# Kernel optimization log

Hardware: AMD Instinct MI355X
Metric: run time of the kernel (lower is better)

Reference implementation:

```python
import jax, jax.numpy as jnp
import numpy as np

N = 50000      # nodes
E = 1600000    # edges (avg degree 32)
F_IN = 3       # PROTEINS num_node_features
H = 64         # dim_h
G = 512        # num graphs in batch
C = 2          # PROTEINS num_classes
BN_EPS = 1e-5


def setup_inputs() -> dict:
    key = jax.random.key(0)
    ks = iter(jax.random.split(key, 64))

    def rn(shape, s=0.1):
        return (jax.random.normal(next(ks), shape) * s).astype(jnp.float32)

    inp = {"x": rn((N, F_IN), 1.0)}
    for li, din in ((1, F_IN), (2, H), (3, H)):
        p = f"conv{li}_"
        inp[p + "w1"] = rn((din, H))
        inp[p + "b1"] = rn((H,))
        inp[p + "bn_g"] = jnp.ones((H,), jnp.float32)
        inp[p + "bn_b"] = jnp.zeros((H,), jnp.float32)
        inp[p + "bn_m"] = rn((H,))
        inp[p + "bn_v"] = jax.random.uniform(next(ks), (H,), jnp.float32, 0.5, 1.5)
        inp[p + "w2"] = rn((H, H))
        inp[p + "b2"] = rn((H,))
    inp["lin1_w"] = rn((3 * H, 3 * H))
    inp["lin1_b"] = rn((3 * H,))
    inp["lin2_w"] = rn((3 * H, C))
    inp["lin2_b"] = rn((C,))
    inp["edge_index"] = jax.random.randint(next(ks), (2, E), 0, N, jnp.int64)
    inp["batch"] = jnp.sort(jax.random.randint(next(ks), (N,), 0, G, jnp.int64))
    return inp


def gin_conv(x, src, dst, w1, b1, g, bb, m, v, w2, b2):
    # GINConv, eps=0: mlp(x + sum_{j->i} x_j); aggregate messages at target (dst)
    agg = jax.ops.segment_sum(x[src], dst, num_segments=N)  # [N, d]
    h = x + agg
    h = h @ w1 + b1
    h = (h - m) * jax.lax.rsqrt(v + BN_EPS) * g + bb  # BatchNorm1d (eval)
    h = jax.nn.relu(h)
    h = jax.nn.relu(h @ w2 + b2)
    return h


def reference(x,
              conv1_w1, conv1_b1, conv1_bn_g, conv1_bn_b, conv1_bn_m, conv1_bn_v, conv1_w2, conv1_b2,
              conv2_w1, conv2_b1, conv2_bn_g, conv2_bn_b, conv2_bn_m, conv2_bn_v, conv2_w2, conv2_b2,
              conv3_w1, conv3_b1, conv3_bn_g, conv3_bn_b, conv3_bn_m, conv3_bn_v, conv3_w2, conv3_b2,
              lin1_w, lin1_b, lin2_w, lin2_b,
              edge_index, batch):
    src, dst = edge_index[0], edge_index[1]
    h1 = gin_conv(x,  src, dst, conv1_w1, conv1_b1, conv1_bn_g, conv1_bn_b, conv1_bn_m, conv1_bn_v, conv1_w2, conv1_b2)
    h2 = gin_conv(h1, src, dst, conv2_w1, conv2_b1, conv2_bn_g, conv2_bn_b, conv2_bn_m, conv2_bn_v, conv2_w2, conv2_b2)
    h3 = gin_conv(h2, src, dst, conv3_w1, conv3_b1, conv3_bn_g, conv3_bn_b, conv3_bn_m, conv3_bn_v, conv3_w2, conv3_b2)
    # global_add_pool per graph
    p1 = jax.ops.segment_sum(h1, batch, num_segments=G)
    p2 = jax.ops.segment_sum(h2, batch, num_segments=G)
    p3 = jax.ops.segment_sum(h3, batch, num_segments=G)
    h = jnp.concatenate((p1, p2, p3), axis=1)          # [G, 3H]
    h = jax.nn.relu(h @ lin1_w + lin1_b)
    # dropout p=0.5 is identity in eval mode
    h = h @ lin2_w + lin2_b                            # [G, C]
    return (h, jax.nn.log_softmax(h, axis=1))
```

## Files before the change

kernel.cpp:

```cpp
#include <hip/hip_runtime.h>
#include <hip/hip_bf16.h>
#include <math.h>

#define N_NODES 50000
#define N_EDGES 1600000
#define H 64
#define G_GRAPHS 512
#define C_CLS 2
#define BN_EPS 1e-5f
#define NBUCK 196
#define BUCKCAP 16384
#define E4 (N_EDGES / 4)
#define CSR_BLOCKS ((E4 + 511) / 512)
#define IOP 72

typedef __attribute__((ext_vector_type(8))) short short8;
typedef __attribute__((ext_vector_type(4))) float floatx4;

__device__ __forceinline__ float bflo(unsigned int u) { return __uint_as_float(u << 16); }
__device__ __forceinline__ float bfhi(unsigned int u) { return __uint_as_float(u & 0xffff0000u); }
__device__ __forceinline__ unsigned int bf16_rne(float f) {
    unsigned int u = __float_as_uint(f);
    u += 0x7fffu + ((u >> 16) & 1u);
    return u >> 16;
}

__global__ __launch_bounds__(256) void prep_kernel(
    const float* __restrict__ w2_0, const float* __restrict__ w1_1,
    const float* __restrict__ w2_1, const float* __restrict__ w1_2,
    const float* __restrict__ w2_2, unsigned short* __restrict__ wt,
    const float* __restrict__ x, uint2* __restrict__ xb) {
    int b = blockIdx.x, t = threadIdx.x;
    if (b < 5) {
        const float* w = (b == 0) ? w2_0 : (b == 1) ? w1_1 : (b == 2) ? w2_1
                         : (b == 3) ? w1_2 : w2_2;
        unsigned short* o = wt + b * (H * H);
        for (int idx = t; idx < H * H; idx += 256) {
            int k = idx >> 6, j = idx & 63;
            o[j * H + k] = (unsigned short)bf16_rne(w[idx]);
        }
    } else {
        int node = (b - 5) * 256 + t;
        if (node < N_NODES) {
            uint2 p;
            p.x = bf16_rne(x[node * 3 + 0]) | (bf16_rne(x[node * 3 + 1]) << 16);
            p.y = bf16_rne(x[node * 3 + 2]);
            xb[node] = p;
        }
    }
}

__global__ __launch_bounds__(256) void scatter1_kernel(const int* __restrict__ src,
                                                       const int* __restrict__ dst,
                                                       int* __restrict__ gcnt,
                                                       int* __restrict__ gpacked) {
    __shared__ int bh[NBUCK];
    int t = threadIdx.x;
    if (t < NBUCK) bh[t] = 0;
    __syncthreads();
    int base = blockIdx.x * 512;

    int pkA[4], bkA[4], lrA[4]; bool vA = false;
    int pkB[4], bkB[4], lrB[4]; bool vB = false;
    {
        int i = base + t;
        if (i < E4) {
            vA = true;
            int4 s4 = ((const int4*)src)[i];
            int4 d4 = ((const int4*)dst)[i];
            bkA[0] = d4.x >> 8; pkA[0] = ((d4.x & 255) << 16) | s4.x; lrA[0] = atomicAdd(&bh[bkA[0]], 1);
            bkA[1] = d4.y >> 8; pkA[1] = ((d4.y & 255) << 16) | s4.y; lrA[1] = atomicAdd(&bh[bkA[1]], 1);
            bkA[2] = d4.z >> 8; pkA[2] = ((d4.z & 255) << 16) | s4.z; lrA[2] = atomicAdd(&bh[bkA[2]], 1);
            bkA[3] = d4.w >> 8; pkA[3] = ((d4.w & 255) << 16) | s4.w; lrA[3] = atomicAdd(&bh[bkA[3]], 1);
        }
    }
    {
        int i = base + 256 + t;
        if (i < E4) {
            vB = true;
            int4 s4 = ((const int4*)src)[i];
            int4 d4 = ((const int4*)dst)[i];
            bkB[0] = d4.x >> 8; pkB[0] = ((d4.x & 255) << 16) | s4.x; lrB[0] = atomicAdd(&bh[bkB[0]], 1);
            bkB[1] = d4.y >> 8; pkB[1] = ((d4.y & 255) << 16) | s4.y; lrB[1] = atomicAdd(&bh[bkB[1]], 1);
            bkB[2] = d4.z >> 8; pkB[2] = ((d4.z & 255) << 16) | s4.z; lrB[2] = atomicAdd(&bh[bkB[2]], 1);
            bkB[3] = d4.w >> 8; pkB[3] = ((d4.w & 255) << 16) | s4.w; lrB[3] = atomicAdd(&bh[bkB[3]], 1);
        }
    }
    __syncthreads();
    if (t < NBUCK) {
        int c = bh[t];
        bh[t] = c ? atomicAdd(&gcnt[t], c) : 0;
    }
    __syncthreads();
    if (vA) {
#pragma unroll
        for (int q = 0; q < 4; q++) gpacked[bkA[q] * BUCKCAP + bh[bkA[q]] + lrA[q]] = pkA[q];
    }
    if (vB) {
#pragma unroll
        for (int q = 0; q < 4; q++) gpacked[bkB[q] * BUCKCAP + bh[bkB[q]] + lrB[q]] = pkB[q];
    }
}

__global__ __launch_bounds__(256) void bcsr_kernel(const int* __restrict__ gpacked,
                                                   const int* __restrict__ gcnt,
                                                   int* __restrict__ row_start,
                                                   int* __restrict__ edge_src) {
    __shared__ int cnt[256];
    __shared__ int pref[256];
    int b = blockIdx.x;
    int t = threadIdx.x;

    int v = (t < NBUCK) ? gcnt[t] : 0;
    pref[t] = v;
    __syncthreads();
    for (int off = 1; off < 256; off <<= 1) {
        int u = 0;
        if (t >= off) u = pref[t - off];
        __syncthreads();
        if (t >= off) pref[t] += u;
        __syncthreads();
    }
    int bs = (b > 0) ? pref[b - 1] : 0;
    int cnt_b = gcnt[b];
    if (b == 0 && t == 0) row_start[N_NODES] = N_EDGES;
    __syncthreads();

    const int* gp = gpacked + (size_t)b * BUCKCAP;
    cnt[t] = 0;
    __syncthreads();
    for (int i = t; i < cnt_b; i += 256) atomicAdd(&cnt[gp[i] >> 16], 1);
    __syncthreads();
    int c = cnt[t];
    pref[t] = c;
    __syncthreads();
    for (int off = 1; off < 256; off <<= 1) {
        int u = 0;
        if (t >= off) u = pref[t - off];
        __syncthreads();
        if (t >= off) pref[t] += u;
        __syncthreads();
    }
    int excl = pref[t] - c;
    int node = b * 256 + t;
    if (node < N_NODES) row_start[node] = bs + excl;
    cnt[t] = excl;
    __syncthreads();
    for (int i = t; i < cnt_b; i += 256) {
        int p = gp[i];
        int pos = atomicAdd(&cnt[p >> 16], 1);
        edge_src[bs + pos] = p & 0xffff;
    }
}

__global__ __launch_bounds__(512) void gin1_fused16_kernel(
    const float* __restrict__ x, const uint2* __restrict__ xb,
    const int* __restrict__ row_start, const int* __restrict__ edge_src,
    const float* __restrict__ w1, const float* __restrict__ b1,
    const float* __restrict__ bn_g, const float* __restrict__ bn_b,
    const float* __restrict__ bn_m, const float* __restrict__ bn_v,
    const unsigned short* __restrict__ w2t, const float* __restrict__ b2,
    __hip_bfloat16* __restrict__ hout) {
    __shared__ unsigned short s_mid[16 * IOP];

    int tid = threadIdx.x;
    int wave = tid >> 6, j = tid & 63;
    int nodebase = blockIdx.x * 16;

    float wj0 = w1[j], wj1 = w1[H + j], wj2 = w1[2 * H + j];
    float sc = rsqrtf(bn_v[j] + BN_EPS) * bn_g[j];
    float sh = bn_b[j] - bn_m[j] * sc;
    float bj = b1[j];

    for (int nl = wave * 2; nl < wave * 2 + 2; nl++) {
        int node = nodebase + nl;
        int rs = row_start[node], re = row_start[node + 1];
        float a0 = 0.f, a1 = 0.f, a2 = 0.f;
        for (int t = rs + j; t < re; t += 64) {
            uint2 p = xb[edge_src[t]];
            a0 += bflo(p.x); a1 += bfhi(p.x); a2 += bflo(p.y);
        }
#pragma unroll
        for (int off = 32; off > 0; off >>= 1) {
            a0 += __shfl_xor(a0, off);
            a1 += __shfl_xor(a1, off);
            a2 += __shfl_xor(a2, off);
        }
        float in0 = a0 + x[node * 3 + 0];
        float in1 = a1 + x[node * 3 + 1];
        float in2 = a2 + x[node * 3 + 2];
        float m = bj + in0 * wj0 + in1 * wj1 + in2 * wj2;
        m = fmaxf(m * sc + sh, 0.f);
        s_mid[nl * IOP + j] = (unsigned short)bf16_rne(m);
    }
    __syncthreads();

    if (wave == 0) {
        int quad = j >> 4, l15 = j & 15;
        float bb2[4];
#pragma unroll
        for (int jt = 0; jt < 4; jt++) bb2[jt] = b2[jt * 16 + l15];

        short8 m0 = *(const short8*)&s_mid[l15 * IOP + quad * 8];
        short8 m1 = *(const short8*)&s_mid[l15 * IOP + quad * 8 + 32];
#pragma unroll
        for (int jt = 0; jt < 4; jt++) {
            short8 b0 = *(const short8*)&w2t[(jt * 16 + l15) * H + quad * 8];
            short8 bv = *(const short8*)&w2t[(jt * 16 + l15) * H + quad * 8 + 32];
            floatx4 c = {0.f, 0.f, 0.f, 0.f};
            c = __builtin_amdgcn_mfma_f32_16x16x32_bf16(m0, b0, c, 0, 0, 0);
            c = __builtin_amdgcn_mfma_f32_16x16x32_bf16(m1, bv, c, 0, 0, 0);
#pragma unroll
            for (int r = 0; r < 4; r++) {
                float v = fmaxf(c[r] + bb2[jt], 0.f);
                s_mid[(quad * 4 + r) * IOP + jt * 16 + l15] = (unsigned short)bf16_rne(v);
            }
        }
        unsigned short* ho = (unsigned short*)hout;
#pragma unroll
        for (int cc = 0; cc < 2; cc++) {
            int r = cc * 8 + (j >> 3);
            short8 v = *(const short8*)&s_mid[r * IOP + (j & 7) * 8];
            *(short8*)(ho + (size_t)(nodebase + r) * H + (j & 7) * 8) = v;
        }
    }
}

__global__ __launch_bounds__(512) void gin_fused16_kernel(
    const __hip_bfloat16* __restrict__ hin, const int* __restrict__ row_start,
    const int* __restrict__ edge_src,
    const unsigned short* __restrict__ w1t, const float* __restrict__ b1,
    const float* __restrict__ bn_g, const float* __restrict__ bn_b,
    const float* __restrict__ bn_m, const float* __restrict__ bn_v,
    const unsigned short* __restrict__ w2t, const float* __restrict__ b2,
    __hip_bfloat16* __restrict__ hout) {
    __shared__ unsigned short s_xs[16 * IOP];
    __shared__ unsigned short s_mid[16 * IOP];

    int tid = threadIdx.x;
    int wave = tid >> 6, j = tid & 63;
    int o = j >> 3, jo = j & 7;
    int nodebase = blockIdx.x * 16;

    const char* hb = (const char*)hin;

    for (int nl = wave * 2; nl < wave * 2 + 2; nl++) {
        int node = nodebase + nl;
        int rs = row_start[node], re = row_start[node + 1];
        float a0 = 0.f, a1 = 0.f, a2 = 0.f, a3 = 0.f, a4 = 0.f, a5 = 0.f, a6 = 0.f, a7 = 0.f;
        float b0 = 0.f, b1v = 0.f, b2v = 0.f, b3 = 0.f, b4 = 0.f, b5 = 0.f, b6 = 0.f, b7 = 0.f;
        for (int base = rs; base < re; base += 64) {
            int idx = base + j;
            int sv = (idx < re) ? edge_src[idx] : 0;
            int cnt = min(64, re - base);
            int i = 0;
            for (; i + 16 <= cnt; i += 16) {
                int s0 = __shfl(sv, i + o);
                int s1 = __shfl(sv, i + 8 + o);
                uint4 r0 = *(const uint4*)(hb + (size_t)s0 * 128 + jo * 16);
                uint4 r1 = *(const uint4*)(hb + (size_t)s1 * 128 + jo * 16);
                a0 += bflo(r0.x); a1 += bfhi(r0.x);
                a2 += bflo(r0.y); a3 += bfhi(r0.y);
                a4 += bflo(r0.z); a5 += bfhi(r0.z);
                a6 += bflo(r0.w); a7 += bfhi(r0.w);
                b0 += bflo(r1.x); b1v += bfhi(r1.x);
                b2v += bflo(r1.y); b3 += bfhi(r1.y);
                b4 += bflo(r1.z); b5 += bfhi(r1.z);
                b6 += bflo(r1.w); b7 += bfhi(r1.w);
            }
            for (; i + 8 <= cnt; i += 8) {
                int s = __shfl(sv, i + o);
                uint4 raw = *(const uint4*)(hb + (size_t)s * 128 + jo * 16);
                a0 += bflo(raw.x); a1 += bfhi(raw.x);
                a2 += bflo(raw.y); a3 += bfhi(raw.y);
                a4 += bflo(raw.z); a5 += bfhi(raw.z);
                a6 += bflo(raw.w); a7 += bfhi(raw.w);
            }
            if (i < cnt) {
                int r = cnt - i;
                int s = __shfl(sv, i + (o < r ? o : 0));
                uint4 raw = *(const uint4*)(hb + (size_t)s * 128 + jo * 16);
                if (o < r) {
                    a0 += bflo(raw.x); a1 += bfhi(raw.x);
                    a2 += bflo(raw.y); a3 += bfhi(raw.y);
                    a4 += bflo(raw.z); a5 += bfhi(raw.z);
                    a6 += bflo(raw.w); a7 += bfhi(raw.w);
                }
            }
        }
        a0 += b0; a1 += b1v; a2 += b2v; a3 += b3;
        a4 += b4; a5 += b5; a6 += b6; a7 += b7;
        a0 += __shfl_xor(a0, 8); a0 += __shfl_xor(a0, 16); a0 += __shfl_xor(a0, 32);
        a1 += __shfl_xor(a1, 8); a1 += __shfl_xor(a1, 16); a1 += __shfl_xor(a1, 32);
        a2 += __shfl_xor(a2, 8); a2 += __shfl_xor(a2, 16); a2 += __shfl_xor(a2, 32);
        a3 += __shfl_xor(a3, 8); a3 += __shfl_xor(a3, 16); a3 += __shfl_xor(a3, 32);
        a4 += __shfl_xor(a4, 8); a4 += __shfl_xor(a4, 16); a4 += __shfl_xor(a4, 32);
        a5 += __shfl_xor(a5, 8); a5 += __shfl_xor(a5, 16); a5 += __shfl_xor(a5, 32);
        a6 += __shfl_xor(a6, 8); a6 += __shfl_xor(a6, 16); a6 += __shfl_xor(a6, 32);
        a7 += __shfl_xor(a7, 8); a7 += __shfl_xor(a7, 16); a7 += __shfl_xor(a7, 32);
        if (o == 0) {
            uint4 raw = *(const uint4*)(hb + (size_t)node * 128 + jo * 16);
            a0 += bflo(raw.x); a1 += bfhi(raw.x);
            a2 += bflo(raw.y); a3 += bfhi(raw.y);
            a4 += bflo(raw.z); a5 += bfhi(raw.z);
            a6 += bflo(raw.w); a7 += bfhi(raw.w);
            uint4 ov;
            ov.x = bf16_rne(a0) | (bf16_rne(a1) << 16);
            ov.y = bf16_rne(a2) | (bf16_rne(a3) << 16);
            ov.z = bf16_rne(a4) | (bf16_rne(a5) << 16);
            ov.w = bf16_rne(a6) | (bf16_rne(a7) << 16);
            *(uint4*)&s_xs[nl * IOP + jo * 8] = ov;
        }
    }
    __syncthreads();

    if (wave == 0) {
        int quad = j >> 4, l15 = j & 15;
        float scl[4], sht[4], bb1[4], bb2[4];
#pragma unroll
        for (int jt = 0; jt < 4; jt++) {
            int jj = jt * 16 + l15;
            float sc = rsqrtf(bn_v[jj] + BN_EPS) * bn_g[jj];
            scl[jt] = sc;
            sht[jt] = bn_b[jj] - bn_m[jj] * sc;
            bb1[jt] = b1[jj];
            bb2[jt] = b2[jj];
        }
        short8 a0 = *(const short8*)&s_xs[l15 * IOP + quad * 8];
        short8 a1 = *(const short8*)&s_xs[l15 * IOP + quad * 8 + 32];
#pragma unroll
        for (int jt = 0; jt < 4; jt++) {
            short8 b0 = *(const short8*)&w1t[(jt * 16 + l15) * H + quad * 8];
            short8 bv = *(const short8*)&w1t[(jt * 16 + l15) * H + quad * 8 + 32];
            floatx4 c = {0.f, 0.f, 0.f, 0.f};
            c = __builtin_amdgcn_mfma_f32_16x16x32_bf16(a0, b0, c, 0, 0, 0);
            c = __builtin_amdgcn_mfma_f32_16x16x32_bf16(a1, bv, c, 0, 0, 0);
#pragma unroll
            for (int r = 0; r < 4; r++) {
                float v = (c[r] + bb1[jt]) * scl[jt] + sht[jt];
                v = fmaxf(v, 0.f);
                s_mid[(quad * 4 + r) * IOP + jt * 16 + l15] = (unsigned short)bf16_rne(v);
            }
        }
        short8 m0 = *(const short8*)&s_mid[l15 * IOP + quad * 8];
        short8 m1 = *(const short8*)&s_mid[l15 * IOP + quad * 8 + 32];
#pragma unroll
        for (int jt = 0; jt < 4; jt++) {
            short8 b0 = *(const short8*)&w2t[(jt * 16 + l15) * H + quad * 8];
            short8 bv = *(const short8*)&w2t[(jt * 16 + l15) * H + quad * 8 + 32];
            floatx4 c = {0.f, 0.f, 0.f, 0.f};
            c = __builtin_amdgcn_mfma_f32_16x16x32_bf16(m0, b0, c, 0, 0, 0);
            c = __builtin_amdgcn_mfma_f32_16x16x32_bf16(m1, bv, c, 0, 0, 0);
#pragma unroll
            for (int r = 0; r < 4; r++) {
                float v = fmaxf(c[r] + bb2[jt], 0.f);
                s_xs[(quad * 4 + r) * IOP + jt * 16 + l15] = (unsigned short)bf16_rne(v);
            }
        }
        unsigned short* ho = (unsigned short*)hout;
#pragma unroll
        for (int cc = 0; cc < 2; cc++) {
            int r = cc * 8 + (j >> 3);
            short8 v = *(const short8*)&s_xs[r * IOP + (j & 7) * 8];
            *(short8*)(ho + (size_t)(nodebase + r) * H + (j & 7) * 8) = v;
        }
    }
}

__global__ __launch_bounds__(192) void pool_head_kernel(
    const __hip_bfloat16* __restrict__ h1, const __hip_bfloat16* __restrict__ h2,
    const __hip_bfloat16* __restrict__ h3, const int* __restrict__ batch,
    const float* __restrict__ lin1_w, const float* __restrict__ lin1_b,
    const float* __restrict__ lin2_w, const float* __restrict__ lin2_b,
    float* __restrict__ out) {
    __shared__ float s_row[3 * H];
    __shared__ float s_mid[3 * H];
    __shared__ float s_z[C_CLS];
    __shared__ int s_se[2];

    int g = blockIdx.x;
    int j = threadIdx.x;
    if (j < 2) {
        int target = g + j;
        int lo = 0, hi = N_NODES;
        while (lo < hi) {
            int mid = (lo + hi) >> 1;
            if (batch[mid] < target) lo = mid + 1; else hi = mid;
        }
        s_se[j] = lo;
    }
    __syncthreads();
    int ns = s_se[0], ne = s_se[1];

    int which = j >> 6;
    int f = j & 63;
    const __hip_bfloat16* h = (which == 0) ? h1 : ((which == 1) ? h2 : h3);
    float p0 = 0.f, p1 = 0.f, p2 = 0.f, p3 = 0.f;
    int n = ns;
    for (; n + 3 < ne; n += 4) {
        p0 += __bfloat162float(h[(size_t)n * H + f]);
        p1 += __bfloat162float(h[(size_t)(n + 1) * H + f]);
        p2 += __bfloat162float(h[(size_t)(n + 2) * H + f]);
        p3 += __bfloat162float(h[(size_t)(n + 3) * H + f]);
    }
    for (; n < ne; n++) p0 += __bfloat162float(h[(size_t)n * H + f]);
    s_row[j] = (p0 + p1) + (p2 + p3);
    __syncthreads();

    float acc = lin1_b[j];
    for (int k = 0; k < 3 * H; k++) acc += s_row[k] * lin1_w[k * (3 * H) + j];
    s_mid[j] = fmaxf(acc, 0.f);
    __syncthreads();

    if (j < C_CLS) {
        float z = lin2_b[j];
        for (int k = 0; k < 3 * H; k++) z += s_mid[k] * lin2_w[k * C_CLS + j];
        s_z[j] = z;
    }
    __syncthreads();
    if (j < C_CLS) {
        float z0 = s_z[0], z1 = s_z[1];
        float mx = fmaxf(z0, z1);
        float lse = mx + logf(expf(z0 - mx) + expf(z1 - mx));
        out[g * C_CLS + j] = s_z[j];
        out[G_GRAPHS * C_CLS + g * C_CLS + j] = s_z[j] - lse;
    }
}

extern "C" void kernel_launch(void* const* d_in, const int* in_sizes, int n_in,
                              void* d_out, int out_size, void* d_ws, size_t ws_size,
                              hipStream_t stream) {
    const float* x = (const float*)d_in[0];
    const float* cw1[3], *cb1[3], *cg[3], *cbb[3], *cm[3], *cv[3], *cw2[3], *cb2[3];
    for (int l = 0; l < 3; l++) {
        int b = 1 + 8 * l;
        cw1[l] = (const float*)d_in[b + 0];
        cb1[l] = (const float*)d_in[b + 1];
        cg[l]  = (const float*)d_in[b + 2];
        cbb[l] = (const float*)d_in[b + 3];
        cm[l]  = (const float*)d_in[b + 4];
        cv[l]  = (const float*)d_in[b + 5];
        cw2[l] = (const float*)d_in[b + 6];
        cb2[l] = (const float*)d_in[b + 7];
    }
    const float* lin1_w = (const float*)d_in[25];
    const float* lin1_b = (const float*)d_in[26];
    const float* lin2_w = (const float*)d_in[27];
    const float* lin2_b = (const float*)d_in[28];
    const int* edge_index = (const int*)d_in[29];
    const int* batch = (const int*)d_in[30];
    const int* src = edge_index;
    const int* dst = edge_index + N_EDGES;
    float* out = (float*)d_out;

    int* edge_src = (int*)d_ws;
    int* gpacked = edge_src + N_EDGES;
    int* gcnt = gpacked + (size_t)NBUCK * BUCKCAP;
    int* row_start = gcnt + NBUCK;
    uintptr_t hp = (uintptr_t)(row_start + N_NODES + 2);
    hp = (hp + 127) & ~(uintptr_t)127;
    unsigned short* wt = (unsigned short*)hp;
    uint2* xb = (uint2*)(wt + 5 * H * H);
    __hip_bfloat16* h1 = (__hip_bfloat16*)(xb + N_NODES);
    __hip_bfloat16* h2 = h1 + (size_t)N_NODES * H;
    __hip_bfloat16* h3 = h2 + (size_t)N_NODES * H;

    const unsigned short* w2t_0 = wt + 0 * H * H;
    const unsigned short* w1t_1 = wt + 1 * H * H;
    const unsigned short* w2t_1 = wt + 2 * H * H;
    const unsigned short* w1t_2 = wt + 3 * H * H;
    const unsigned short* w2t_2 = wt + 4 * H * H;

    hipMemsetAsync(gcnt, 0, NBUCK * sizeof(int), stream);
    prep_kernel<<<5 + (N_NODES + 255) / 256, 256, 0, stream>>>(
        cw2[0], cw1[1], cw2[1], cw1[2], cw2[2], wt, x, xb);
    scatter1_kernel<<<CSR_BLOCKS, 256, 0, stream>>>(src, dst, gcnt, gpacked);
    bcsr_kernel<<<NBUCK, 256, 0, stream>>>(gpacked, gcnt, row_start, edge_src);

    const int fgrid = N_NODES / 16;

    gin1_fused16_kernel<<<fgrid, 512, 0, stream>>>(x, xb, row_start, edge_src,
        cw1[0], cb1[0], cg[0], cbb[0], cm[0], cv[0], w2t_0, cb2[0], h1);
    gin_fused16_kernel<<<fgrid, 512, 0, stream>>>(h1, row_start, edge_src,
        w1t_1, cb1[1], cg[1], cbb[1], cm[1], cv[1], w2t_1, cb2[1], h2);
    gin_fused16_kernel<<<fgrid, 512, 0, stream>>>(h2, row_start, edge_src,
        w1t_2, cb1[2], cg[2], cbb[2], cm[2], cv[2], w2t_2, cb2[2], h3);
    pool_head_kernel<<<G_GRAPHS, 3 * H, 0, stream>>>(h1, h2, h3, batch,
        lin1_w, lin1_b, lin2_w, lin2_b, out);
}
```

Before: 281.9 us.

## Merge all stages into one persistent kernel with grid barriers and fused pooling

Replaces the seven separate launches (prep, scatter, CSR build, three GIN layers, pool/head) with one persistent kernel of 768 blocks. Stages are separated by a software grid barrier built on atomics. Global add pooling now happens inside each GIN layer through a batch lookup and atomic accumulation into a pool buffer, which removes the separate pass that re-read h1, h2 and h3. The gather loop is also restructured: blocks use 256 threads, each wave handles 4 nodes, and 4 gathers are in flight per step. This cuts launch gaps and redundant reads, but adds barrier spin cost, assumes all 768 blocks are co-resident, and lowers per-block parallelism.

```diff
diff --git a/kernel.cpp b/kernel.cpp
--- a/kernel.cpp
+++ b/kernel.cpp
@@ -11,8 +11,12 @@
 #define NBUCK 196
 #define BUCKCAP 16384
 #define E4 (N_EDGES / 4)
-#define CSR_BLOCKS ((E4 + 511) / 512)
+#define SCHUNKS ((E4 + 511) / 512)
+#define XCHUNKS ((N_NODES + 255) / 256)
+#define P0_UNITS (SCHUNKS + 5 + XCHUNKS)
+#define NGROUP (N_NODES / 16)
 #define IOP 72
+#define GRID 768
 
 typedef __attribute__((ext_vector_type(8))) short short8;
 typedef __attribute__((ext_vector_type(4))) float floatx4;
@@ -25,279 +29,72 @@
     return u >> 16;
 }
 
-__global__ __launch_bounds__(256) void prep_kernel(
-    const float* __restrict__ w2_0, const float* __restrict__ w1_1,
-    const float* __restrict__ w2_1, const float* __restrict__ w1_2,
-    const float* __restrict__ w2_2, unsigned short* __restrict__ wt,
-    const float* __restrict__ x, uint2* __restrict__ xb) {
-    int b = blockIdx.x, t = threadIdx.x;
-    if (b < 5) {
-        const float* w = (b == 0) ? w2_0 : (b == 1) ? w1_1 : (b == 2) ? w2_1
-                         : (b == 3) ? w1_2 : w2_2;
-        unsigned short* o = wt + b * (H * H);
-        for (int idx = t; idx < H * H; idx += 256) {
-            int k = idx >> 6, j = idx & 63;
-            o[j * H + k] = (unsigned short)bf16_rne(w[idx]);
-        }
-    } else {
-        int node = (b - 5) * 256 + t;
-        if (node < N_NODES) {
-            uint2 p;
-            p.x = bf16_rne(x[node * 3 + 0]) | (bf16_rne(x[node * 3 + 1]) << 16);
-            p.y = bf16_rne(x[node * 3 + 2]);
-            xb[node] = p;
-        }
-    }
-}
-
-__global__ __launch_bounds__(256) void scatter1_kernel(const int* __restrict__ src,
-                                                       const int* __restrict__ dst,
-                                                       int* __restrict__ gcnt,
-                                                       int* __restrict__ gpacked) {
-    __shared__ int bh[NBUCK];
-    int t = threadIdx.x;
-    if (t < NBUCK) bh[t] = 0;
-    __syncthreads();
-    int base = blockIdx.x * 512;
-
-    int pkA[4], bkA[4], lrA[4]; bool vA = false;
-    int pkB[4], bkB[4], lrB[4]; bool vB = false;
-    {
-        int i = base + t;
-        if (i < E4) {
-            vA = true;
-            int4 s4 = ((const int4*)src)[i];
-            int4 d4 = ((const int4*)dst)[i];
-            bkA[0] = d4.x >> 8; pkA[0] = ((d4.x & 255) << 16) | s4.x; lrA[0] = atomicAdd(&bh[bkA[0]], 1);
-            bkA[1] = d4.y >> 8; pkA[1] = ((d4.y & 255) << 16) | s4.y; lrA[1] = atomicAdd(&bh[bkA[1]], 1);
-            bkA[2] = d4.z >> 8; pkA[2] = ((d4.z & 255) << 16) | s4.z; lrA[2] = atomicAdd(&bh[bkA[2]], 1);
-            bkA[3] = d4.w >> 8; pkA[3] = ((d4.w & 255) << 16) | s4.w; lrA[3] = atomicAdd(&bh[bkA[3]], 1);
-        }
-    }
-    {
-        int i = base + 256 + t;
-        if (i < E4) {
-            vB = true;
-            int4 s4 = ((const int4*)src)[i];
-            int4 d4 = ((const int4*)dst)[i];
-            bkB[0] = d4.x >> 8; pkB[0] = ((d4.x & 255) << 16) | s4.x; lrB[0] = atomicAdd(&bh[bkB[0]], 1);
-            bkB[1] = d4.y >> 8; pkB[1] = ((d4.y & 255) << 16) | s4.y; lrB[1] = atomicAdd(&bh[bkB[1]], 1);
-            bkB[2] = d4.z >> 8; pkB[2] = ((d4.z & 255) << 16) | s4.z; lrB[2] = atomicAdd(&bh[bkB[2]], 1);
-            bkB[3] = d4.w >> 8; pkB[3] = ((d4.w & 255) << 16) | s4.w; lrB[3] = atomicAdd(&bh[bkB[3]], 1);
-        }
-    }
-    __syncthreads();
-    if (t < NBUCK) {
-        int c = bh[t];
-        bh[t] = c ? atomicAdd(&gcnt[t], c) : 0;
-    }
-    __syncthreads();
-    if (vA) {
-#pragma unroll
-        for (int q = 0; q < 4; q++) gpacked[bkA[q] * BUCKCAP + bh[bkA[q]] + lrA[q]] = pkA[q];
-    }
-    if (vB) {
-#pragma unroll
-        for (int q = 0; q < 4; q++) gpacked[bkB[q] * BUCKCAP + bh[bkB[q]] + lrB[q]] = pkB[q];
-    }
-}
-
-__global__ __launch_bounds__(256) void bcsr_kernel(const int* __restrict__ gpacked,
-                                                   const int* __restrict__ gcnt,
-                                                   int* __restrict__ row_start,
-                                                   int* __restrict__ edge_src) {
-    __shared__ int cnt[256];
-    __shared__ int pref[256];
-    int b = blockIdx.x;
-    int t = threadIdx.x;
-
-    int v = (t < NBUCK) ? gcnt[t] : 0;
-    pref[t] = v;
-    __syncthreads();
-    for (int off = 1; off < 256; off <<= 1) {
-        int u = 0;
-        if (t >= off) u = pref[t - off];
-        __syncthreads();
-        if (t >= off) pref[t] += u;
-        __syncthreads();
-    }
-    int bs = (b > 0) ? pref[b - 1] : 0;
-    int cnt_b = gcnt[b];
-    if (b == 0 && t == 0) row_start[N_NODES] = N_EDGES;
-    __syncthreads();
-
-    const int* gp = gpacked + (size_t)b * BUCKCAP;
-    cnt[t] = 0;
-    __syncthreads();
-    for (int i = t; i < cnt_b; i += 256) atomicAdd(&cnt[gp[i] >> 16], 1);
-    __syncthreads();
-    int c = cnt[t];
-    pref[t] = c;
-    __syncthreads();
-    for (int off = 1; off < 256; off <<= 1) {
-        int u = 0;
-        if (t >= off) u = pref[t - off];
-        __syncthreads();
-        if (t >= off) pref[t] += u;
-        __syncthreads();
-    }
-    int excl = pref[t] - c;
-    int node = b * 256 + t;
-    if (node < N_NODES) row_start[node] = bs + excl;
-    cnt[t] = excl;
-    __syncthreads();
-    for (int i = t; i < cnt_b; i += 256) {
-        int p = gp[i];
-        int pos = atomicAdd(&cnt[p >> 16], 1);
-        edge_src[bs + pos] = p & 0xffff;
-    }
-}
-
-__global__ __launch_bounds__(512) void gin1_fused16_kernel(
-    const float* __restrict__ x, const uint2* __restrict__ xb,
-    const int* __restrict__ row_start, const int* __restrict__ edge_src,
-    const float* __restrict__ w1, const float* __restrict__ b1,
-    const float* __restrict__ bn_g, const float* __restrict__ bn_b,
-    const float* __restrict__ bn_m, const float* __restrict__ bn_v,
-    const unsigned short* __restrict__ w2t, const float* __restrict__ b2,
+#define RED3(A) { A += __shfl_xor(A, 8); A += __shfl_xor(A, 16); A += __shfl_xor(A, 32); }
+#define RED6(A) { A += __shfl_xor(A, 1); A += __shfl_xor(A, 2); A += __shfl_xor(A, 4); \
+                  A += __shfl_xor(A, 8); A += __shfl_xor(A, 16); A += __shfl_xor(A, 32); }
+
+__device__ __forceinline__ void gbar(int* bar) {
+    __syncthreads();
+    if (threadIdx.x == 0) {
+        __threadfence();
+        int g = __hip_atomic_load(&bar[1], __ATOMIC_RELAXED, __HIP_MEMORY_SCOPE_AGENT);
+        int a = __hip_atomic_fetch_add(&bar[0], 1, __ATOMIC_ACQ_REL, __HIP_MEMORY_SCOPE_AGENT);
+        if (a == GRID - 1) {
+            __hip_atomic_store(&bar[0], 0, __ATOMIC_RELAXED, __HIP_MEMORY_SCOPE_AGENT);
+            __hip_atomic_store(&bar[1], g + 1, __ATOMIC_RELEASE, __HIP_MEMORY_SCOPE_AGENT);
+        } else {
+            while (__hip_atomic_load(&bar[1], __ATOMIC_RELAXED, __HIP_MEMORY_SCOPE_AGENT) == g)
+                __builtin_amdgcn_s_sleep(1);
+        }
+        __threadfence();
+    }
+    __syncthreads();
+}
+
+#define ACCV(R) { \
+    a0 += bflo(R.x); a1 += bfhi(R.x); a2 += bflo(R.y); a3 += bfhi(R.y); \
+    a4 += bflo(R.z); a5 += bfhi(R.z); a6 += bflo(R.w); a7 += bfhi(R.w); }
+
+__device__ __forceinline__ void gin_group(
+    int nodebase, int wave, int j, int quad, int l15, int jj,
+    const char* hb, const int* __restrict__ row_start, const int* __restrict__ edge_src,
+    short8 wb10, short8 wb11, short8 wb20, short8 wb21,
+    float sc, float sh, float bb1, float bb2,
+    unsigned short* s_xs, unsigned short* s_mid, int* s_bat,
+    const int* __restrict__ batch, float* __restrict__ poolcol,
     __hip_bfloat16* __restrict__ hout) {
-    __shared__ unsigned short s_mid[16 * IOP];
-
-    int tid = threadIdx.x;
-    int wave = tid >> 6, j = tid & 63;
-    int nodebase = blockIdx.x * 16;
-
-    float wj0 = w1[j], wj1 = w1[H + j], wj2 = w1[2 * H + j];
-    float sc = rsqrtf(bn_v[j] + BN_EPS) * bn_g[j];
-    float sh = bn_b[j] - bn_m[j] * sc;
-    float bj = b1[j];
-
-    for (int nl = wave * 2; nl < wave * 2 + 2; nl++) {
+    int o = j >> 3, jo = j & 7;
+    if (wave == 0 && j < 16) s_bat[j] = batch[nodebase + j];
+
+    for (int q = 0; q < 4; q++) {
+        int nl = wave * 4 + q;
         int node = nodebase + nl;
         int rs = row_start[node], re = row_start[node + 1];
-        float a0 = 0.f, a1 = 0.f, a2 = 0.f;
-        for (int t = rs + j; t < re; t += 64) {
-            uint2 p = xb[edge_src[t]];
-            a0 += bflo(p.x); a1 += bfhi(p.x); a2 += bflo(p.y);
-        }
-#pragma unroll
-        for (int off = 32; off > 0; off >>= 1) {
-            a0 += __shfl_xor(a0, off);
-            a1 += __shfl_xor(a1, off);
-            a2 += __shfl_xor(a2, off);
-        }
-        float in0 = a0 + x[node * 3 + 0];
-        float in1 = a1 + x[node * 3 + 1];
-        float in2 = a2 + x[node * 3 + 2];
-        float m = bj + in0 * wj0 + in1 * wj1 + in2 * wj2;
-        m = fmaxf(m * sc + sh, 0.f);
-        s_mid[nl * IOP + j] = (unsigned short)bf16_rne(m);
-    }
-    __syncthreads();
-
-    if (wave == 0) {
-        int quad = j >> 4, l15 = j & 15;
-        float bb2[4];
-#pragma unroll
-        for (int jt = 0; jt < 4; jt++) bb2[jt] = b2[jt * 16 + l15];
-
-        short8 m0 = *(const short8*)&s_mid[l15 * IOP + quad * 8];
-        short8 m1 = *(const short8*)&s_mid[l15 * IOP + quad * 8 + 32];
-#pragma unroll
-        for (int jt = 0; jt < 4; jt++) {
-            short8 b0 = *(const short8*)&w2t[(jt * 16 + l15) * H + quad * 8];
-            short8 bv = *(const short8*)&w2t[(jt * 16 + l15) * H + quad * 8 + 32];
-            floatx4 c = {0.f, 0.f, 0.f, 0.f};
-            c = __builtin_amdgcn_mfma_f32_16x16x32_bf16(m0, b0, c, 0, 0, 0);
-            c = __builtin_amdgcn_mfma_f32_16x16x32_bf16(m1, bv, c, 0, 0, 0);
-#pragma unroll
-            for (int r = 0; r < 4; r++) {
-                float v = fmaxf(c[r] + bb2[jt], 0.f);
-                s_mid[(quad * 4 + r) * IOP + jt * 16 + l15] = (unsigned short)bf16_rne(v);
-            }
-        }
-        unsigned short* ho = (unsigned short*)hout;
-#pragma unroll
-        for (int cc = 0; cc < 2; cc++) {
-            int r = cc * 8 + (j >> 3);
-            short8 v = *(const short8*)&s_mid[r * IOP + (j & 7) * 8];
-            *(short8*)(ho + (size_t)(nodebase + r) * H + (j & 7) * 8) = v;
-        }
-    }
-}
-
-__global__ __launch_bounds__(512) void gin_fused16_kernel(
-    const __hip_bfloat16* __restrict__ hin, const int* __restrict__ row_start,
-    const int* __restrict__ edge_src,
-    const unsigned short* __restrict__ w1t, const float* __restrict__ b1,
-    const float* __restrict__ bn_g, const float* __restrict__ bn_b,
-    const float* __restrict__ bn_m, const float* __restrict__ bn_v,
-    const unsigned short* __restrict__ w2t, const float* __restrict__ b2,
-    __hip_bfloat16* __restrict__ hout) {
-    __shared__ unsigned short s_xs[16 * IOP];
-    __shared__ unsigned short s_mid[16 * IOP];
-
-    int tid = threadIdx.x;
-    int wave = tid >> 6, j = tid & 63;
-    int o = j >> 3, jo = j & 7;
-    int nodebase = blockIdx.x * 16;
-
-    const char* hb = (const char*)hin;
-
-    for (int nl = wave * 2; nl < wave * 2 + 2; nl++) {
-        int node = nodebase + nl;
-        int rs = row_start[node], re = row_start[node + 1];
+        int cntv = re - rs;
         float a0 = 0.f, a1 = 0.f, a2 = 0.f, a3 = 0.f, a4 = 0.f, a5 = 0.f, a6 = 0.f, a7 = 0.f;
-        float b0 = 0.f, b1v = 0.f, b2v = 0.f, b3 = 0.f, b4 = 0.f, b5 = 0.f, b6 = 0.f, b7 = 0.f;
-        for (int base = rs; base < re; base += 64) {
-            int idx = base + j;
+        for (int base = 0; base < cntv; base += 64) {
+            int idx = rs + base + j;
             int sv = (idx < re) ? edge_src[idx] : 0;
-            int cnt = min(64, re - base);
-            int i = 0;
-            for (; i + 16 <= cnt; i += 16) {
-                int s0 = __shfl(sv, i + o);
-                int s1 = __shfl(sv, i + 8 + o);
-                uint4 r0 = *(const uint4*)(hb + (size_t)s0 * 128 + jo * 16);
-                uint4 r1 = *(const uint4*)(hb + (size_t)s1 * 128 + jo * 16);
-                a0 += bflo(r0.x); a1 += bfhi(r0.x);
-                a2 += bflo(r0.y); a3 += bfhi(r0.y);
-                a4 += bflo(r0.z); a5 += bfhi(r0.z);
-                a6 += bflo(r0.w); a7 += bfhi(r0.w);
-                b0 += bflo(r1.x); b1v += bfhi(r1.x);
-                b2v += bflo(r1.y); b3 += bfhi(r1.y);
-                b4 += bflo(r1.z); b5 += bfhi(r1.z);
-                b6 += bflo(r1.w); b7 += bfhi(r1.w);
-            }
-            for (; i + 8 <= cnt; i += 8) {
-                int s = __shfl(sv, i + o);
-                uint4 raw = *(const uint4*)(hb + (size_t)s * 128 + jo * 16);
-                a0 += bflo(raw.x); a1 += bfhi(raw.x);
-                a2 += bflo(raw.y); a3 += bfhi(raw.y);
-                a4 += bflo(raw.z); a5 += bfhi(raw.z);
-                a6 += bflo(raw.w); a7 += bfhi(raw.w);
-            }
-            if (i < cnt) {
-                int r = cnt - i;
-                int s = __shfl(sv, i + (o < r ? o : 0));
-                uint4 raw = *(const uint4*)(hb + (size_t)s * 128 + jo * 16);
-                if (o < r) {
-                    a0 += bflo(raw.x); a1 += bfhi(raw.x);
-                    a2 += bflo(raw.y); a3 += bfhi(raw.y);
-                    a4 += bflo(raw.z); a5 += bfhi(raw.z);
-                    a6 += bflo(raw.w); a7 += bfhi(raw.w);
-                }
-            }
-        }
-        a0 += b0; a1 += b1v; a2 += b2v; a3 += b3;
-        a4 += b4; a5 += b5; a6 += b6; a7 += b7;
-        a0 += __shfl_xor(a0, 8); a0 += __shfl_xor(a0, 16); a0 += __shfl_xor(a0, 32);
-        a1 += __shfl_xor(a1, 8); a1 += __shfl_xor(a1, 16); a1 += __shfl_xor(a1, 32);
-        a2 += __shfl_xor(a2, 8); a2 += __shfl_xor(a2, 16); a2 += __shfl_xor(a2, 32);
-        a3 += __shfl_xor(a3, 8); a3 += __shfl_xor(a3, 16); a3 += __shfl_xor(a3, 32);
-        a4 += __shfl_xor(a4, 8); a4 += __shfl_xor(a4, 16); a4 += __shfl_xor(a4, 32);
-        a5 += __shfl_xor(a5, 8); a5 += __shfl_xor(a5, 16); a5 += __shfl_xor(a5, 32);
-        a6 += __shfl_xor(a6, 8); a6 += __shfl_xor(a6, 16); a6 += __shfl_xor(a6, 32);
-        a7 += __shfl_xor(a7, 8); a7 += __shfl_xor(a7, 16); a7 += __shfl_xor(a7, 32);
+            int lim = min(64, cntv - base);
+#pragma unroll
+            for (int i = 0; i < 64; i += 32) {
+                if (i >= lim) break;
+                int r0 = i + o, r1 = i + 8 + o, r2 = i + 16 + o, r3 = i + 24 + o;
+                int s0 = __shfl(sv, r0);
+                int s1 = __shfl(sv, r1);
+                int s2 = __shfl(sv, r2);
+                int s3 = __shfl(sv, r3);
+                uint4 R0 = *(const uint4*)(hb + (size_t)s0 * 128 + jo * 16);
+                uint4 R1 = *(const uint4*)(hb + (size_t)s1 * 128 + jo * 16);
+                uint4 R2 = *(const uint4*)(hb + (size_t)s2 * 128 + jo * 16);
+                uint4 R3 = *(const uint4*)(hb + (size_t)s3 * 128 + jo * 16);
+                if (r0 < lim) ACCV(R0)
+                if (r1 < lim) ACCV(R1)
+                if (r2 < lim) ACCV(R2)
+                if (r3 < lim) ACCV(R3)
+            }
+        }
+        RED3(a0) RED3(a1) RED3(a2) RED3(a3) RED3(a4) RED3(a5) RED3(a6) RED3(a7)
         if (o == 0) {
             uint4 raw = *(const uint4*)(hb + (size_t)node * 128 + jo * 16);
             a0 += bflo(raw.x); a1 += bfhi(raw.x);
@@ -314,116 +111,335 @@
     }
     __syncthreads();
 
-    if (wave == 0) {
-        int quad = j >> 4, l15 = j & 15;
-        float scl[4], sht[4], bb1[4], bb2[4];
-#pragma unroll
-        for (int jt = 0; jt < 4; jt++) {
-            int jj = jt * 16 + l15;
-            float sc = rsqrtf(bn_v[jj] + BN_EPS) * bn_g[jj];
-            scl[jt] = sc;
-            sht[jt] = bn_b[jj] - bn_m[jj] * sc;
-            bb1[jt] = b1[jj];
-            bb2[jt] = b2[jj];
-        }
-        short8 a0 = *(const short8*)&s_xs[l15 * IOP + quad * 8];
-        short8 a1 = *(const short8*)&s_xs[l15 * IOP + quad * 8 + 32];
-#pragma unroll
-        for (int jt = 0; jt < 4; jt++) {
-            short8 b0 = *(const short8*)&w1t[(jt * 16 + l15) * H + quad * 8];
-            short8 bv = *(const short8*)&w1t[(jt * 16 + l15) * H + quad * 8 + 32];
-            floatx4 c = {0.f, 0.f, 0.f, 0.f};
-            c = __builtin_amdgcn_mfma_f32_16x16x32_bf16(a0, b0, c, 0, 0, 0);
-            c = __builtin_amdgcn_mfma_f32_16x16x32_bf16(a1, bv, c, 0, 0, 0);
-#pragma unroll
-            for (int r = 0; r < 4; r++) {
-                float v = (c[r] + bb1[jt]) * scl[jt] + sht[jt];
-                v = fmaxf(v, 0.f);
-                s_mid[(quad * 4 + r) * IOP + jt * 16 + l15] = (unsigned short)bf16_rne(v);
-            }
-        }
-        short8 m0 = *(const short8*)&s_mid[l15 * IOP + quad * 8];
-        short8 m1 = *(const short8*)&s_mid[l15 * IOP + quad * 8 + 32];
-#pragma unroll
-        for (int jt = 0; jt < 4; jt++) {
-            short8 b0 = *(const short8*)&w2t[(jt * 16 + l15) * H + quad * 8];
-            short8 bv = *(const short8*)&w2t[(jt * 16 + l15) * H + quad * 8 + 32];
-            floatx4 c = {0.f, 0.f, 0.f, 0.f};
-            c = __builtin_amdgcn_mfma_f32_16x16x32_bf16(m0, b0, c, 0, 0, 0);
-            c = __builtin_amdgcn_mfma_f32_16x16x32_bf16(m1, bv, c, 0, 0, 0);
-#pragma unroll
-            for (int r = 0; r < 4; r++) {
-                float v = fmaxf(c[r] + bb2[jt], 0.f);
-                s_xs[(quad * 4 + r) * IOP + jt * 16 + l15] = (unsigned short)bf16_rne(v);
-            }
-        }
-        unsigned short* ho = (unsigned short*)hout;
-#pragma unroll
-        for (int cc = 0; cc < 2; cc++) {
-            int r = cc * 8 + (j >> 3);
-            short8 v = *(const short8*)&s_xs[r * IOP + (j & 7) * 8];
-            *(short8*)(ho + (size_t)(nodebase + r) * H + (j & 7) * 8) = v;
-        }
-    }
-}
-
-__global__ __launch_bounds__(192) void pool_head_kernel(
-    const __hip_bfloat16* __restrict__ h1, const __hip_bfloat16* __restrict__ h2,
-    const __hip_bfloat16* __restrict__ h3, const int* __restrict__ batch,
+    {
+        short8 A0 = *(const short8*)&s_xs[l15 * IOP + quad * 8];
+        short8 A1 = *(const short8*)&s_xs[l15 * IOP + quad * 8 + 32];
+        floatx4 c = {0.f, 0.f, 0.f, 0.f};
+        c = __builtin_amdgcn_mfma_f32_16x16x32_bf16(A0, wb10, c, 0, 0, 0);
+        c = __builtin_amdgcn_mfma_f32_16x16x32_bf16(A1, wb11, c, 0, 0, 0);
+#pragma unroll
+        for (int r = 0; r < 4; r++) {
+            float v = (c[r] + bb1) * sc + sh;
+            v = fmaxf(v, 0.f);
+            s_mid[(quad * 4 + r) * IOP + jj] = (unsigned short)bf16_rne(v);
+        }
+    }
+    __syncthreads();
+
+    {
+        short8 M0 = *(const short8*)&s_mid[l15 * IOP + quad * 8];
+        short8 M1 = *(const short8*)&s_mid[l15 * IOP + quad * 8 + 32];
+        floatx4 c = {0.f, 0.f, 0.f, 0.f};
+        c = __builtin_amdgcn_mfma_f32_16x16x32_bf16(M0, wb20, c, 0, 0, 0);
+        c = __builtin_amdgcn_mfma_f32_16x16x32_bf16(M1, wb21, c, 0, 0, 0);
+        float vv[4];
+#pragma unroll
+        for (int r = 0; r < 4; r++) {
+            vv[r] = fmaxf(c[r] + bb2, 0.f);
+            s_xs[(quad * 4 + r) * IOP + jj] = (unsigned short)bf16_rne(vv[r]);
+        }
+        int bq0 = s_bat[quad * 4], bq3 = s_bat[quad * 4 + 3];
+        if (bq0 == bq3) {
+            atomicAdd(&poolcol[bq0 * 192 + jj], (vv[0] + vv[1]) + (vv[2] + vv[3]));
+        } else {
+            atomicAdd(&poolcol[s_bat[quad * 4 + 0] * 192 + jj], vv[0]);
+            atomicAdd(&poolcol[s_bat[quad * 4 + 1] * 192 + jj], vv[1]);
+            atomicAdd(&poolcol[s_bat[quad * 4 + 2] * 192 + jj], vv[2]);
+            atomicAdd(&poolcol[s_bat[quad * 4 + 3] * 192 + jj], vv[3]);
+        }
+    }
+    __syncthreads();
+
+    if (j < 32) {
+        int r = wave * 4 + (j >> 3), ch = j & 7;
+        short8 v = *(const short8*)&s_xs[r * IOP + ch * 8];
+        *(short8*)((unsigned short*)hout + (size_t)(nodebase + r) * H + ch * 8) = v;
+    }
+    __syncthreads();
+}
+
+__device__ __forceinline__ void gin1_group(
+    int nodebase, int wave, int j, int quad, int l15, int jj,
+    const float* __restrict__ x, const uint2* __restrict__ xb,
+    const int* __restrict__ row_start, const int* __restrict__ edge_src,
+    float wj0, float wj1, float wj2, float sc1, float sh1, float bj,
+    short8 wb20, short8 wb21, float bb2,
+    unsigned short* s_xs, unsigned short* s_mid, int* s_bat,
+    const int* __restrict__ batch, float* __restrict__ poolcol,
+    __hip_bfloat16* __restrict__ hout) {
+    if (wave == 0 && j < 16) s_bat[j] = batch[nodebase + j];
+
+    for (int q = 0; q < 4; q++) {
+        int nl = wave * 4 + q;
+        int node = nodebase + nl;
+        int rs = row_start[node], re = row_start[node + 1];
+        float a0 = 0.f, a1 = 0.f, a2 = 0.f;
+        for (int t2 = rs + j; t2 < re; t2 += 64) {
+            uint2 p = xb[edge_src[t2]];
+            a0 += bflo(p.x); a1 += bfhi(p.x); a2 += bflo(p.y);
+        }
+        RED6(a0) RED6(a1) RED6(a2)
+        float in0 = a0 + x[node * 3 + 0];
+        float in1 = a1 + x[node * 3 + 1];
+        float in2 = a2 + x[node * 3 + 2];
+        float m = bj + in0 * wj0 + in1 * wj1 + in2 * wj2;
+        m = fmaxf(m * sc1 + sh1, 0.f);
+        s_mid[nl * IOP + j] = (unsigned short)bf16_rne(m);
+    }
+    __syncthreads();
+
+    {
+        short8 M0 = *(const short8*)&s_mid[l15 * IOP + quad * 8];
+        short8 M1 = *(const short8*)&s_mid[l15 * IOP + quad * 8 + 32];
+        floatx4 c = {0.f, 0.f, 0.f, 0.f};
+        c = __builtin_amdgcn_mfma_f32_16x16x32_bf16(M0, wb20, c, 0, 0, 0);
+        c = __builtin_amdgcn_mfma_f32_16x16x32_bf16(M1, wb21, c, 0, 0, 0);
+        float vv[4];
+#pragma unroll
+        for (int r = 0; r < 4; r++) {
+            vv[r] = fmaxf(c[r] + bb2, 0.f);
+            s_xs[(quad * 4 + r) * IOP + jj] = (unsigned short)bf16_rne(vv[r]);
+        }
+        int bq0 = s_bat[quad * 4], bq3 = s_bat[quad * 4 + 3];
+        if (bq0 == bq3) {
+            atomicAdd(&poolcol[bq0 * 192 + jj], (vv[0] + vv[1]) + (vv[2] + vv[3]));
+        } else {
+            atomicAdd(&poolcol[s_bat[quad * 4 + 0] * 192 + jj], vv[0]);
+            atomicAdd(&poolcol[s_bat[quad * 4 + 1] * 192 + jj], vv[1]);
+            atomicAdd(&poolcol[s_bat[quad * 4 + 2] * 192 + jj], vv[2]);
+            atomicAdd(&poolcol[s_bat[quad * 4 + 3] * 192 + jj], vv[3]);
+        }
+    }
+    __syncthreads();
+
+    if (j < 32) {
+        int r = wave * 4 + (j >> 3), ch = j & 7;
+        short8 v = *(const short8*)&s_xs[r * IOP + ch * 8];
+        *(short8*)((unsigned short*)hout + (size_t)(nodebase + r) * H + ch * 8) = v;
+    }
+    __syncthreads();
+}
+
+__global__ __launch_bounds__(256, 4) void mega_kernel(
+    const float* __restrict__ x,
+    const float* __restrict__ w1_0, const float* __restrict__ b1_0,
+    const float* __restrict__ g_0, const float* __restrict__ bb_0,
+    const float* __restrict__ m_0, const float* __restrict__ v_0,
+    const float* __restrict__ w2_0f, const float* __restrict__ b2_0,
+    const float* __restrict__ w1_1f, const float* __restrict__ b1_1,
+    const float* __restrict__ g_1, const float* __restrict__ bb_1,
+    const float* __restrict__ m_1, const float* __restrict__ v_1,
+    const float* __restrict__ w2_1f, const float* __restrict__ b2_1,
+    const float* __restrict__ w1_2f, const float* __restrict__ b1_2,
+    const float* __restrict__ g_2, const float* __restrict__ bb_2,
+    const float* __restrict__ m_2, const float* __restrict__ v_2,
+    const float* __restrict__ w2_2f, const float* __restrict__ b2_2,
     const float* __restrict__ lin1_w, const float* __restrict__ lin1_b,
     const float* __restrict__ lin2_w, const float* __restrict__ lin2_b,
-    float* __restrict__ out) {
-    __shared__ float s_row[3 * H];
-    __shared__ float s_mid[3 * H];
+    const int* __restrict__ esrc, const int* __restrict__ edst,
+    const int* __restrict__ batch,
+    int* __restrict__ edge_src, int* __restrict__ gpacked, int* __restrict__ gcnt,
+    int* bar, float* __restrict__ pool, int* __restrict__ row_start,
+    unsigned short* __restrict__ wt, uint2* __restrict__ xb,
+    __hip_bfloat16* __restrict__ h1, __hip_bfloat16* __restrict__ h2,
+    __hip_bfloat16* __restrict__ h3, float* __restrict__ out) {
+    __shared__ int s_ia[256];
+    __shared__ int s_ib[256];
+    __shared__ unsigned short s_xs[16 * IOP];
+    __shared__ unsigned short s_mid[16 * IOP];
+    __shared__ int s_bat[16];
+    __shared__ float s_hr[192];
+    __shared__ float s_hm[192];
     __shared__ float s_z[C_CLS];
-    __shared__ int s_se[2];
-
-    int g = blockIdx.x;
-    int j = threadIdx.x;
-    if (j < 2) {
-        int target = g + j;
-        int lo = 0, hi = N_NODES;
-        while (lo < hi) {
-            int mid = (lo + hi) >> 1;
-            if (batch[mid] < target) lo = mid + 1; else hi = mid;
-        }
-        s_se[j] = lo;
-    }
-    __syncthreads();
-    int ns = s_se[0], ne = s_se[1];
-
-    int which = j >> 6;
-    int f = j & 63;
-    const __hip_bfloat16* h = (which == 0) ? h1 : ((which == 1) ? h2 : h3);
-    float p0 = 0.f, p1 = 0.f, p2 = 0.f, p3 = 0.f;
-    int n = ns;
-    for (; n + 3 < ne; n += 4) {
-        p0 += __bfloat162float(h[(size_t)n * H + f]);
-        p1 += __bfloat162float(h[(size_t)(n + 1) * H + f]);
-        p2 += __bfloat162float(h[(size_t)(n + 2) * H + f]);
-        p3 += __bfloat162float(h[(size_t)(n + 3) * H + f]);
-    }
-    for (; n < ne; n++) p0 += __bfloat162float(h[(size_t)n * H + f]);
-    s_row[j] = (p0 + p1) + (p2 + p3);
-    __syncthreads();
-
-    float acc = lin1_b[j];
-    for (int k = 0; k < 3 * H; k++) acc += s_row[k] * lin1_w[k * (3 * H) + j];
-    s_mid[j] = fmaxf(acc, 0.f);
-    __syncthreads();
-
-    if (j < C_CLS) {
-        float z = lin2_b[j];
-        for (int k = 0; k < 3 * H; k++) z += s_mid[k] * lin2_w[k * C_CLS + j];
-        s_z[j] = z;
-    }
-    __syncthreads();
-    if (j < C_CLS) {
-        float z0 = s_z[0], z1 = s_z[1];
-        float mx = fmaxf(z0, z1);
-        float lse = mx + logf(expf(z0 - mx) + expf(z1 - mx));
-        out[g * C_CLS + j] = s_z[j];
-        out[G_GRAPHS * C_CLS + g * C_CLS + j] = s_z[j] - lse;
+
+    int t = threadIdx.x;
+    int wave = t >> 6, j = t & 63;
+    int quad = j >> 4, l15 = j & 15;
+    int jj = wave * 16 + l15;
+
+    for (int u = blockIdx.x; u < P0_UNITS; u += GRID) {
+        if (u < SCHUNKS) {
+            int base = u * 512;
+            if (t < NBUCK) s_ia[t] = 0;
+            __syncthreads();
+            int pkA[4], bkA[4], lrA[4]; bool vA = false;
+            int pkB[4], bkB[4], lrB[4]; bool vB = false;
+            {
+                int i = base + t;
+                if (i < E4) {
+                    vA = true;
+                    int4 s4 = ((const int4*)esrc)[i];
+                    int4 d4 = ((const int4*)edst)[i];
+                    bkA[0] = d4.x >> 8; pkA[0] = ((d4.x & 255) << 16) | s4.x; lrA[0] = atomicAdd(&s_ia[bkA[0]], 1);
+                    bkA[1] = d4.y >> 8; pkA[1] = ((d4.y & 255) << 16) | s4.y; lrA[1] = atomicAdd(&s_ia[bkA[1]], 1);
+                    bkA[2] = d4.z >> 8; pkA[2] = ((d4.z & 255) << 16) | s4.z; lrA[2] = atomicAdd(&s_ia[bkA[2]], 1);
+                    bkA[3] = d4.w >> 8; pkA[3] = ((d4.w & 255) << 16) | s4.w; lrA[3] = atomicAdd(&s_ia[bkA[3]], 1);
+                }
+            }
+            {
+                int i = base + 256 + t;
+                if (i < E4) {
+                    vB = true;
+                    int4 s4 = ((const int4*)esrc)[i];
+                    int4 d4 = ((const int4*)edst)[i];
+                    bkB[0] = d4.x >> 8; pkB[0] = ((d4.x & 255) << 16) | s4.x; lrB[0] = atomicAdd(&s_ia[bkB[0]], 1);
+                    bkB[1] = d4.y >> 8; pkB[1] = ((d4.y & 255) << 16) | s4.y; lrB[1] = atomicAdd(&s_ia[bkB[1]], 1);
+                    bkB[2] = d4.z >> 8; pkB[2] = ((d4.z & 255) << 16) | s4.z; lrB[2] = atomicAdd(&s_ia[bkB[2]], 1);
+                    bkB[3] = d4.w >> 8; pkB[3] = ((d4.w & 255) << 16) | s4.w; lrB[3] = atomicAdd(&s_ia[bkB[3]], 1);
+                }
+            }
+            __syncthreads();
+            if (t < NBUCK) {
+                int c = s_ia[t];
+                s_ia[t] = c ? atomicAdd(&gcnt[t], c) : 0;
+            }
+            __syncthreads();
+            if (vA) {
+#pragma unroll
+                for (int q = 0; q < 4; q++) gpacked[bkA[q] * BUCKCAP + s_ia[bkA[q]] + lrA[q]] = pkA[q];
+            }
+            if (vB) {
+#pragma unroll
+                for (int q = 0; q < 4; q++) gpacked[bkB[q] * BUCKCAP + s_ia[bkB[q]] + lrB[q]] = pkB[q];
+            }
+            __syncthreads();
+        } else if (u < SCHUNKS + 5) {
+            int b = u - SCHUNKS;
+            const float* w = (b == 0) ? w2_0f : (b == 1) ? w1_1f : (b == 2) ? w2_1f
+                             : (b == 3) ? w1_2f : w2_2f;
+            unsigned short* ow = wt + b * (H * H);
+            for (int idx = t; idx < H * H; idx += 256) {
+                int k = idx >> 6, jc = idx & 63;
+                ow[jc * H + k] = (unsigned short)bf16_rne(w[idx]);
+            }
+        } else {
+            int node = (u - SCHUNKS - 5) * 256 + t;
+            if (node < N_NODES) {
+                uint2 p;
+                p.x = bf16_rne(x[node * 3 + 0]) | (bf16_rne(x[node * 3 + 1]) << 16);
+                p.y = bf16_rne(x[node * 3 + 2]);
+                xb[node] = p;
+            }
+        }
+    }
+    gbar(bar);
+
+    if (blockIdx.x == 0 && t == 0) row_start[N_NODES] = N_EDGES;
+    if (blockIdx.x < NBUCK) {
+        int b = blockIdx.x;
+        int v = (t < NBUCK) ? gcnt[t] : 0;
+        s_ib[t] = v;
+        __syncthreads();
+        for (int off = 1; off < 256; off <<= 1) {
+            int u2 = 0;
+            if (t >= off) u2 = s_ib[t - off];
+            __syncthreads();
+            if (t >= off) s_ib[t] += u2;
+            __syncthreads();
+        }
+        int bs = (b > 0) ? s_ib[b - 1] : 0;
+        int cnt_b = gcnt[b];
+        const int* gp = gpacked + (size_t)b * BUCKCAP;
+        s_ia[t] = 0;
+        __syncthreads();
+        for (int i = t; i < cnt_b; i += 256) atomicAdd(&s_ia[gp[i] >> 16], 1);
+        __syncthreads();
+        int c = s_ia[t];
+        s_ib[t] = c;
+        __syncthreads();
+        for (int off = 1; off < 256; off <<= 1) {
+            int u2 = 0;
+            if (t >= off) u2 = s_ib[t - off];
+            __syncthreads();
+            if (t >= off) s_ib[t] += u2;
+            __syncthreads();
+        }
+        int excl = s_ib[t] - c;
+        int node = b * 256 + t;
+        if (node < N_NODES) row_start[node] = bs + excl;
+        s_ia[t] = excl;
+        __syncthreads();
+        for (int i = t; i < cnt_b; i += 256) {
+            int p = gp[i];
+            int pos = atomicAdd(&s_ia[p >> 16], 1);
+            edge_src[bs + pos] = p & 0xffff;
+        }
+    }
+    gbar(bar);
+
+    {
+        const unsigned short* w2t_0 = wt;
+        float wj0 = w1_0[j], wj1 = w1_0[H + j], wj2 = w1_0[2 * H + j];
+        float sc1 = rsqrtf(v_0[j] + BN_EPS) * g_0[j];
+        float sh1 = bb_0[j] - m_0[j] * sc1;
+        float bj = b1_0[j];
+        short8 wb20 = *(const short8*)&w2t_0[jj * H + quad * 8];
+        short8 wb21 = *(const short8*)&w2t_0[jj * H + quad * 8 + 32];
+        float bb2 = b2_0[jj];
+        for (int grp = blockIdx.x; grp < NGROUP; grp += GRID)
+            gin1_group(grp * 16, wave, j, quad, l15, jj, x, xb, row_start, edge_src,
+                       wj0, wj1, wj2, sc1, sh1, bj, wb20, wb21, bb2,
+                       s_xs, s_mid, s_bat, batch, pool, h1);
+    }
+    gbar(bar);
+
+    {
+        const unsigned short* w1t = wt + 1 * H * H;
+        const unsigned short* w2t = wt + 2 * H * H;
+        float sc = rsqrtf(v_1[jj] + BN_EPS) * g_1[jj];
+        float sh = bb_1[jj] - m_1[jj] * sc;
+        float bb1 = b1_1[jj], bb2 = b2_1[jj];
+        short8 wb10 = *(const short8*)&w1t[jj * H + quad * 8];
+        short8 wb11 = *(const short8*)&w1t[jj * H + quad * 8 + 32];
+        short8 wb20 = *(const short8*)&w2t[jj * H + quad * 8];
+        short8 wb21 = *(const short8*)&w2t[jj * H + quad * 8 + 32];
+        for (int grp = blockIdx.x; grp < NGROUP; grp += GRID)
+            gin_group(grp * 16, wave, j, quad, l15, jj, (const char*)h1, row_start, edge_src,
+                      wb10, wb11, wb20, wb21, sc, sh, bb1, bb2,
+                      s_xs, s_mid, s_bat, batch, pool + 64, h2);
+    }
+    gbar(bar);
+
+    {
+        const unsigned short* w1t = wt + 3 * H * H;
+        const unsigned short* w2t = wt + 4 * H * H;
+        float sc = rsqrtf(v_2[jj] + BN_EPS) * g_2[jj];
+        float sh = bb_2[jj] - m_2[jj] * sc;
+        float bb1 = b1_2[jj], bb2 = b2_2[jj];
+        short8 wb10 = *(const short8*)&w1t[jj * H + quad * 8];
+        short8 wb11 = *(const short8*)&w1t[jj * H + quad * 8 + 32];
+        short8 wb20 = *(const short8*)&w2t[jj * H + quad * 8];
+        short8 wb21 = *(const short8*)&w2t[jj * H + quad * 8 + 32];
+        for (int grp = blockIdx.x; grp < NGROUP; grp += GRID)
+            gin_group(grp * 16, wave, j, quad, l15, jj, (const char*)h2, row_start, edge_src,
+                      wb10, wb11, wb20, wb21, sc, sh, bb1, bb2,
+                      s_xs, s_mid, s_bat, batch, pool + 128, h3);
+    }
+    gbar(bar);
+
+    for (int g = blockIdx.x; g < G_GRAPHS; g += GRID) {
+        if (t < 3 * H) s_hr[t] = pool[g * 192 + t];
+        __syncthreads();
+        if (t < 3 * H) {
+            float acc = lin1_b[t];
+            for (int k = 0; k < 3 * H; k++) acc += s_hr[k] * lin1_w[k * (3 * H) + t];
+            s_hm[t] = fmaxf(acc, 0.f);
+        }
+        __syncthreads();
+        if (t < C_CLS) {
+            float z = lin2_b[t];
+            for (int k = 0; k < 3 * H; k++) z += s_hm[k] * lin2_w[k * C_CLS + t];
+            s_z[t] = z;
+        }
+        __syncthreads();
+        if (t < C_CLS) {
+            float z0 = s_z[0], z1 = s_z[1];
+            float mx = fmaxf(z0, z1);
+            float lse = mx + logf(expf(z0 - mx) + expf(z1 - mx));
+            out[g * C_CLS + t] = s_z[t];
+            out[G_GRAPHS * C_CLS + g * C_CLS + t] = s_z[t] - lse;
+        }
+        __syncthreads();
     }
 }
 
@@ -449,14 +465,16 @@
     const float* lin2_b = (const float*)d_in[28];
     const int* edge_index = (const int*)d_in[29];
     const int* batch = (const int*)d_in[30];
-    const int* src = edge_index;
-    const int* dst = edge_index + N_EDGES;
+    const int* esrc = edge_index;
+    const int* edst = edge_index + N_EDGES;
     float* out = (float*)d_out;
 
     int* edge_src = (int*)d_ws;
     int* gpacked = edge_src + N_EDGES;
     int* gcnt = gpacked + (size_t)NBUCK * BUCKCAP;
-    int* row_start = gcnt + NBUCK;
+    int* bar = gcnt + NBUCK;
+    float* pool = (float*)(bar + 2);
+    int* row_start = (int*)(pool + G_GRAPHS * 3 * H);
     uintptr_t hp = (uintptr_t)(row_start + N_NODES + 2);
     hp = (hp + 127) & ~(uintptr_t)127;
     unsigned short* wt = (unsigned short*)hp;
@@ -465,26 +483,16 @@
     __hip_bfloat16* h2 = h1 + (size_t)N_NODES * H;
     __hip_bfloat16* h3 = h2 + (size_t)N_NODES * H;
 
-    const unsigned short* w2t_0 = wt + 0 * H * H;
-    const unsigned short* w1t_1 = wt + 1 * H * H;
-    const unsigned short* w2t_1 = wt + 2 * H * H;
-    const unsigned short* w1t_2 = wt + 3 * H * H;
-    const unsigned short* w2t_2 = wt + 4 * H * H;
-
-    hipMemsetAsync(gcnt, 0, NBUCK * sizeof(int), stream);
-    prep_kernel<<<5 + (N_NODES + 255) / 256, 256, 0, stream>>>(
-        cw2[0], cw1[1], cw2[1], cw1[2], cw2[2], wt, x, xb);
-    scatter1_kernel<<<CSR_BLOCKS, 256, 0, stream>>>(src, dst, gcnt, gpacked);
-    bcsr_kernel<<<NBUCK, 256, 0, stream>>>(gpacked, gcnt, row_start, edge_src);
-
-    const int fgrid = N_NODES / 16;
-
-    gin1_fused16_kernel<<<fgrid, 512, 0, stream>>>(x, xb, row_start, edge_src,
-        cw1[0], cb1[0], cg[0], cbb[0], cm[0], cv[0], w2t_0, cb2[0], h1);
-    gin_fused16_kernel<<<fgrid, 512, 0, stream>>>(h1, row_start, edge_src,
-        w1t_1, cb1[1], cg[1], cbb[1], cm[1], cv[1], w2t_1, cb2[1], h2);
-    gin_fused16_kernel<<<fgrid, 512, 0, stream>>>(h2, row_start, edge_src,
-        w1t_2, cb1[2], cg[2], cbb[2], cm[2], cv[2], w2t_2, cb2[2], h3);
-    pool_head_kernel<<<G_GRAPHS, 3 * H, 0, stream>>>(h1, h2, h3, batch,
-        lin1_w, lin1_b, lin2_w, lin2_b, out);
-}
+    hipMemsetAsync(gcnt, 0,
+                   (NBUCK + 2) * sizeof(int) + (size_t)G_GRAPHS * 3 * H * sizeof(float),
+                   stream);
+    mega_kernel<<<GRID, 256, 0, stream>>>(
+        x,
+        cw1[0], cb1[0], cg[0], cbb[0], cm[0], cv[0], cw2[0], cb2[0],
+        cw1[1], cb1[1], cg[1], cbb[1], cm[1], cv[1], cw2[1], cb2[1],
+        cw1[2], cb1[2], cg[2], cbb[2], cm[2], cv[2], cw2[2], cb2[2],
+        lin1_w, lin1_b, lin2_w, lin2_b,
+        esrc, edst, batch,
+        edge_src, gpacked, gcnt, bar, pool, row_start,
+        wt, xb, h1, h2, h3, out);
+}
```

Result: slower. 900.7 us (+219.5%).
